# Kernel tuning notes

Hardware: AMD Instinct MI355X
Metric: run time of the kernel (lower is better)

The kernel has to match this reference:

```python
import jax, jax.numpy as jnp
import numpy as np

N_NODES = 50000
N_EDGES = 800000


def _gcn_conv(x, W, b, src, dst, deg_inv_sqrt, n_nodes):
    # PyG GCNConv: h = x @ W, then symmetric-normalized sum aggregation
    h = x @ W  # [N, F_out]
    norm = deg_inv_sqrt[src] * deg_inv_sqrt[dst]  # [E_aug]
    msg = h[src] * norm[:, None]  # [E_aug, F_out]
    out = jax.ops.segment_sum(msg, dst, num_segments=n_nodes)
    return out + b


def setup_inputs() -> dict:
    key = jax.random.key(0)
    k1, k2, k3, k4 = jax.random.split(key, 4)
    x = jax.random.normal(k1, (N_NODES, 128), dtype=jnp.float32)
    edge_index = jax.random.randint(k2, (2, N_EDGES), 0, N_NODES, dtype=jnp.int64)
    W1 = jax.random.normal(k3, (128, 64), dtype=jnp.float32) * (1.0 / np.sqrt(128))
    b1 = jnp.zeros((64,), dtype=jnp.float32)
    W2 = jax.random.normal(k4, (64, 32), dtype=jnp.float32) * (1.0 / np.sqrt(64))
    b2 = jnp.zeros((32,), dtype=jnp.float32)
    return {"x": x, "edge_index": edge_index, "W1": W1, "b1": b1, "W2": W2, "b2": b2}


def reference(x, edge_index, W1, b1, W2, b2):
    n_nodes = x.shape[0]
    # add self-loops (PyG GCNConv default)
    loop = jnp.arange(n_nodes, dtype=edge_index.dtype)
    src = jnp.concatenate([edge_index[0], loop])
    dst = jnp.concatenate([edge_index[1], loop])
    # symmetric normalization: deg from target index (gcn_norm)
    deg = jax.ops.segment_sum(jnp.ones_like(dst, dtype=x.dtype), dst, num_segments=n_nodes)
    deg_inv_sqrt = jnp.where(deg > 0, jax.lax.rsqrt(jnp.maximum(deg, 1.0)), 0.0)

    h = _gcn_conv(x, W1, b1, src, dst, deg_inv_sqrt, n_nodes)
    h = jax.nn.relu(h)
    # dropout is identity in eval mode (reference runs inference)
    out = _gcn_conv(h, W2, b2, src, dst, deg_inv_sqrt, n_nodes)
    return out
```

## Files before the change

kernel.cpp:

```cpp
#include <hip/hip_runtime.h>


#define F_IN 128
#define F_MID 64
#define F_OUT 32
#define NBLK 256

#define RFL(x) __builtin_amdgcn_readfirstlane(x)

__global__ __launch_bounds__(256) void k_hist(
    const int* __restrict__ dst, int E, int chunk, int nbuk,
    int* __restrict__ blockHist) {
    __shared__ int cnt[256];
    int t = threadIdx.x;
    cnt[t] = 0;
    __syncthreads();
    int e0 = blockIdx.x * chunk;
    int e1 = min(E, e0 + chunk);
    for (int e = e0 + t; e < e1; e += 256)
        atomicAdd(&cnt[dst[e] >> 8], 1);
    __syncthreads();
    if (t < nbuk) blockHist[blockIdx.x * nbuk + t] = cnt[t];
}

__global__ __launch_bounds__(256) void k_hist_scan(
    const int* __restrict__ blockHist, int nbuk,
    int* __restrict__ blockOff, int* __restrict__ bucketStart) {
    __shared__ int s[256];
    int t = threadIdx.x;
    int total = 0;
    if (t < nbuk)
        for (int blk = 0; blk < NBLK; ++blk) total += blockHist[blk * nbuk + t];
    s[t] = total;
    __syncthreads();
    for (int o = 1; o < 256; o <<= 1) {
        int add = (t >= o) ? s[t - o] : 0;
        __syncthreads();
        s[t] += add;
        __syncthreads();
    }
    int ex = s[t] - total;
    if (t < nbuk) {
        bucketStart[t] = ex;
        if (t == nbuk - 1) bucketStart[nbuk] = s[t];
        int running = ex;
        for (int blk = 0; blk < NBLK; ++blk) {
            blockOff[blk * nbuk + t] = running;
            running += blockHist[blk * nbuk + t];
        }
    }
}

__global__ __launch_bounds__(256) void k_scatter_edges(
    const int* __restrict__ src, const int* __restrict__ dst, int E, int chunk,
    int nbuk, const int* __restrict__ blockOff, int2* __restrict__ esort) {
    __shared__ int off[256];
    int t = threadIdx.x;
    if (t < nbuk) off[t] = blockOff[blockIdx.x * nbuk + t];
    __syncthreads();
    int e0 = blockIdx.x * chunk;
    int e1 = min(E, e0 + chunk);
    for (int e = e0 + t; e < e1; e += 256) {
        int d = dst[e];
        int pos = atomicAdd(&off[d >> 8], 1);
        esort[pos] = make_int2(d, src[e]);
    }
}

__global__ __launch_bounds__(256) void k_bucket_csr(
    const int2* __restrict__ esort, const int* __restrict__ bucketStart, int n,
    int* __restrict__ rowstart, int* __restrict__ deg, float* __restrict__ dis,
    int* __restrict__ col) {
    __shared__ int cnt[256];
    __shared__ int s[256];
    __shared__ int cur[256];
    int b = blockIdx.x;
    int t = threadIdx.x;
    int node0 = b << 8;
    int e0 = bucketStart[b], e1 = bucketStart[b + 1];
    cnt[t] = 0;
    __syncthreads();
    for (int e = e0 + t; e < e1; e += 256)
        atomicAdd(&cnt[esort[e].x & 255], 1);
    __syncthreads();
    int v = cnt[t];
    s[t] = v;
    __syncthreads();
    for (int o = 1; o < 256; o <<= 1) {
        int add = (t >= o) ? s[t - o] : 0;
        __syncthreads();
        s[t] += add;
        __syncthreads();
    }
    int ex = s[t] - v;
    cur[t] = ex;
    int node = node0 + t;
    if (node < n) {
        rowstart[node] = e0 + ex;
        deg[node] = v;
        dis[node] = rsqrtf((float)(v + 1));
    }
    __syncthreads();
    for (int e = e0 + t; e < e1; e += 256) {
        int2 p = esort[e];
        int pos = atomicAdd(&cur[p.x & 255], 1);
        col[e0 + pos] = p.y;
    }
}

__global__ __launch_bounds__(256, 4) void k_gemm1(
    const float* __restrict__ x, const float* __restrict__ W1,
    const float* __restrict__ dis, float* __restrict__ g1, int n) {
    __shared__ float xs[64 * 129];
    int tid  = threadIdx.x;
    int row0 = blockIdx.x * 64;
    for (int i = tid; i < 64 * F_IN; i += 256) {
        int r = i >> 7, k = i & 127;
        int gr = row0 + r;
        xs[r * 129 + k] = (gr < n) ? x[(size_t)gr * F_IN + k] : 0.0f;
    }
    __syncthreads();
    int w = RFL(tid >> 6);
    int r = tid & 63;
    const float4* W4 = (const float4*)W1;
    float4 a0 = {0.f,0.f,0.f,0.f}, a1 = a0, a2 = a0, a3 = a0;
#pragma unroll 4
    for (int k = 0; k < F_IN; ++k) {
        float xv = xs[r * 129 + k];
        float4 w0 = W4[k * 16 + w * 4 + 0];
        float4 w1 = W4[k * 16 + w * 4 + 1];
        float4 w2 = W4[k * 16 + w * 4 + 2];
        float4 w3 = W4[k * 16 + w * 4 + 3];
        a0.x += xv * w0.x; a0.y += xv * w0.y; a0.z += xv * w0.z; a0.w += xv * w0.w;
        a1.x += xv * w1.x; a1.y += xv * w1.y; a1.z += xv * w1.z; a1.w += xv * w1.w;
        a2.x += xv * w2.x; a2.y += xv * w2.y; a2.z += xv * w2.z; a2.w += xv * w2.w;
        a3.x += xv * w3.x; a3.y += xv * w3.y; a3.z += xv * w3.z; a3.w += xv * w3.w;
    }
    int gr = row0 + r;
    if (gr < n) {
        float dv = dis[gr];
        a0.x *= dv; a0.y *= dv; a0.z *= dv; a0.w *= dv;
        a1.x *= dv; a1.y *= dv; a1.z *= dv; a1.w *= dv;
        a2.x *= dv; a2.y *= dv; a2.z *= dv; a2.w *= dv;
        a3.x *= dv; a3.y *= dv; a3.z *= dv; a3.w *= dv;
        float4* o4 = (float4*)&g1[(size_t)gr * F_MID + w * 16];
        o4[0] = a0; o4[1] = a1; o4[2] = a2; o4[3] = a3;
    }
}

__global__ __launch_bounds__(256) void k_gather1(
    const int* __restrict__ rowstart, const int* __restrict__ deg,
    const int* __restrict__ col, const float* __restrict__ g1,
    const float* __restrict__ dis, const float* __restrict__ b1,
    float* __restrict__ h, int n) {
    int wave = RFL(threadIdx.x >> 6);
    int f    = threadIdx.x & 63;
    int d    = blockIdx.x * 4 + wave;
    if (d >= n) return;
    int base = RFL(rowstart[d]);
    int cnt  = RFL(deg[d]);
    float a0 = g1[(size_t)d * F_MID + f];
    float a1 = 0.f, a2 = 0.f, a3 = 0.f, a4 = 0.f, a5 = 0.f, a6 = 0.f, a7 = 0.f;
    int j = 0;
    for (; j + 8 <= cnt; j += 8) {
        int s0 = col[base + j + 0], s1 = col[base + j + 1];
        int s2 = col[base + j + 2], s3 = col[base + j + 3];
        int s4 = col[base + j + 4], s5 = col[base + j + 5];
        int s6 = col[base + j + 6], s7 = col[base + j + 7];
        a0 += g1[(size_t)s0 * F_MID + f];
        a1 += g1[(size_t)s1 * F_MID + f];
        a2 += g1[(size_t)s2 * F_MID + f];
        a3 += g1[(size_t)s3 * F_MID + f];
        a4 += g1[(size_t)s4 * F_MID + f];
        a5 += g1[(size_t)s5 * F_MID + f];
        a6 += g1[(size_t)s6 * F_MID + f];
        a7 += g1[(size_t)s7 * F_MID + f];
    }
    for (; j + 4 <= cnt; j += 4) {
        int s0 = col[base + j + 0], s1 = col[base + j + 1];
        int s2 = col[base + j + 2], s3 = col[base + j + 3];
        a0 += g1[(size_t)s0 * F_MID + f];
        a1 += g1[(size_t)s1 * F_MID + f];
        a2 += g1[(size_t)s2 * F_MID + f];
        a3 += g1[(size_t)s3 * F_MID + f];
    }
    for (; j < cnt; ++j) a0 += g1[(size_t)col[base + j] * F_MID + f];
    float acc = ((a0 + a1) + (a2 + a3)) + ((a4 + a5) + (a6 + a7));
    h[(size_t)d * F_MID + f] = fmaxf(acc * dis[d] + b1[f], 0.0f);
}

__global__ __launch_bounds__(256, 4) void k_gemm2(
    const float* __restrict__ h, const float* __restrict__ W2,
    const float* __restrict__ dis, float* __restrict__ g2, int n) {
    __shared__ float hs[64 * 65];
    int tid  = threadIdx.x;
    int row0 = blockIdx.x * 64;
    for (int i = tid; i < 64 * F_MID; i += 256) {
        int r = i >> 6, k = i & 63;
        int gr = row0 + r;
        hs[r * 65 + k] = (gr < n) ? h[(size_t)gr * F_MID + k] : 0.0f;
    }
    __syncthreads();
    int w = RFL(tid >> 6);
    int r = tid & 63;
    const float4* W4 = (const float4*)W2;
    float4 a0 = {0.f,0.f,0.f,0.f}, a1 = a0;
#pragma unroll 4
    for (int k = 0; k < F_MID; ++k) {
        float hv = hs[r * 65 + k];
        float4 w0 = W4[k * 8 + w * 2 + 0];
        float4 w1 = W4[k * 8 + w * 2 + 1];
        a0.x += hv * w0.x; a0.y += hv * w0.y; a0.z += hv * w0.z; a0.w += hv * w0.w;
        a1.x += hv * w1.x; a1.y += hv * w1.y; a1.z += hv * w1.z; a1.w += hv * w1.w;
    }
    int gr = row0 + r;
    if (gr < n) {
        float dv = dis[gr];
        a0.x *= dv; a0.y *= dv; a0.z *= dv; a0.w *= dv;
        a1.x *= dv; a1.y *= dv; a1.z *= dv; a1.w *= dv;
        float4* o4 = (float4*)&g2[(size_t)gr * F_OUT + w * 8];
        o4[0] = a0; o4[1] = a1;
    }
}

__global__ __launch_bounds__(256) void k_gather2(
    const int* __restrict__ rowstart, const int* __restrict__ deg,
    const int* __restrict__ col, const float* __restrict__ g2,
    const float* __restrict__ dis, const float* __restrict__ b2,
    float* __restrict__ out, int n) {
    int wave = RFL(threadIdx.x >> 6);
    int lane = threadIdx.x & 63;
    int j    = lane & 31;
    int p    = lane >> 5;
    int d    = blockIdx.x * 4 + wave;
    if (d >= n) return;
    int base = RFL(rowstart[d]);
    int cnt  = RFL(deg[d]);
    float a0 = (p == 0) ? g2[(size_t)d * F_OUT + j] : 0.0f;
    float a1 = 0.f, a2 = 0.f, a3 = 0.f;
    int t = 0;
    for (; t + 8 <= cnt; t += 8) {
        int sA0 = col[base + t + 0], sA1 = col[base + t + 1];
        int sB0 = col[base + t + 2], sB1 = col[base + t + 3];
        int sC0 = col[base + t + 4], sC1 = col[base + t + 5];
        int sD0 = col[base + t + 6], sD1 = col[base + t + 7];
        int sA = p ? sA1 : sA0;
        int sB = p ? sB1 : sB0;
        int sC = p ? sC1 : sC0;
        int sD = p ? sD1 : sD0;
        a0 += g2[(size_t)sA * F_OUT + j];
        a1 += g2[(size_t)sB * F_OUT + j];
        a2 += g2[(size_t)sC * F_OUT + j];
        a3 += g2[(size_t)sD * F_OUT + j];
    }
    for (; t + 2 <= cnt; t += 2) {
        int s0 = col[base + t], s1 = col[base + t + 1];
        int s = p ? s1 : s0;
        a0 += g2[(size_t)s * F_OUT + j];
    }
    if (t < cnt) {
        int s = col[base + t];
        if (p == 0) a0 += g2[(size_t)s * F_OUT + j];
    }
    float acc = (a0 + a1) + (a2 + a3);
    acc += __shfl_xor(acc, 32);
    if (p == 0) out[(size_t)d * F_OUT + j] = acc * dis[d] + b2[j];
}

extern "C" void kernel_launch(void* const* d_in, const int* in_sizes, int n_in,
                              void* d_out, int out_size, void* d_ws, size_t ws_size,
                              hipStream_t stream) {
    const float* x  = (const float*)d_in[0];
    const int*   ei = (const int*)d_in[1];
    const float* W1 = (const float*)d_in[2];
    const float* b1 = (const float*)d_in[3];
    const float* W2 = (const float*)d_in[4];
    const float* b2 = (const float*)d_in[5];

    int n = in_sizes[0] / F_IN;
    int E = in_sizes[1] / 2;
    const int* src = ei;
    const int* dst = ei + E;

    int nbuk  = (n + 255) >> 8;
    int chunk = (E + NBLK - 1) / NBLK;

    char* ws = (char*)d_ws;
    size_t off = 0;
    auto alloc = [&](size_t bytes) {
        char* p = ws + off;
        off += (bytes + 255) & ~(size_t)255;
        return p;
    };
    int*   blockHist   = (int*)  alloc((size_t)NBLK * nbuk * 4);
    int*   blockOff    = (int*)  alloc((size_t)NBLK * nbuk * 4);
    int*   bucketStart = (int*)  alloc((size_t)(nbuk + 1) * 4);
    int2*  esort       = (int2*) alloc((size_t)E * 8);
    int*   col         = (int*)  alloc((size_t)E * 4);
    int*   rowstart    = (int*)  alloc((size_t)n * 4);
    int*   deg         = (int*)  alloc((size_t)n * 4);
    float* dis         = (float*)alloc((size_t)n * 4);
    float* g1          = (float*)alloc((size_t)n * F_MID * 4);
    float* h           = (float*)alloc((size_t)n * F_MID * 4);
    float* g2          = (float*)alloc((size_t)n * F_OUT * 4);

    k_hist<<<NBLK, 256, 0, stream>>>(dst, E, chunk, nbuk, blockHist);
    k_hist_scan<<<1, 256, 0, stream>>>(blockHist, nbuk, blockOff, bucketStart);
    k_scatter_edges<<<NBLK, 256, 0, stream>>>(src, dst, E, chunk, nbuk, blockOff, esort);
    k_bucket_csr<<<nbuk, 256, 0, stream>>>(esort, bucketStart, n, rowstart, deg, dis, col);

    k_gemm1<<<(n + 63) / 64, 256, 0, stream>>>(x, W1, dis, g1, n);
    k_gather1<<<(n + 3) / 4, 256, 0, stream>>>(rowstart, deg, col, g1, dis, b1, h, n);
    k_gemm2<<<(n + 63) / 64, 256, 0, stream>>>(h, W2, dis, g2, n);
    k_gather2<<<(n + 3) / 4, 256, 0, stream>>>(rowstart, deg, col, g2, dis, b2,
                                               (float*)d_out, n);
}
```

Before: 208.7 us.

## Parallelize bucket offset scan across blocks instead of single serial block

```diff
diff --git a/kernel.cpp b/kernel.cpp
--- a/kernel.cpp
+++ b/kernel.cpp
@@ -23,15 +23,32 @@
     if (t < nbuk) blockHist[blockIdx.x * nbuk + t] = cnt[t];
 }
 
-__global__ __launch_bounds__(256) void k_hist_scan(
+__global__ __launch_bounds__(NBLK) void k_scan_buckets(
     const int* __restrict__ blockHist, int nbuk,
-    int* __restrict__ blockOff, int* __restrict__ bucketStart) {
+    int* __restrict__ blockOff, int* __restrict__ bucketTotal) {
+    __shared__ int s[NBLK];
+    int b = blockIdx.x;
+    int t = threadIdx.x;
+    int v = blockHist[t * nbuk + b];
+    s[t] = v;
+    __syncthreads();
+    for (int o = 1; o < NBLK; o <<= 1) {
+        int add = (t >= o) ? s[t - o] : 0;
+        __syncthreads();
+        s[t] += add;
+        __syncthreads();
+    }
+    blockOff[t * nbuk + b] = s[t] - v;
+    if (t == NBLK - 1) bucketTotal[b] = s[t];
+}
+
+__global__ __launch_bounds__(256) void k_scan_starts(
+    const int* __restrict__ bucketTotal, int nbuk, int E,
+    int* __restrict__ bucketStart) {
     __shared__ int s[256];
     int t = threadIdx.x;
-    int total = 0;
-    if (t < nbuk)
-        for (int blk = 0; blk < NBLK; ++blk) total += blockHist[blk * nbuk + t];
-    s[t] = total;
+    int v = (t < nbuk) ? bucketTotal[t] : 0;
+    s[t] = v;
     __syncthreads();
     for (int o = 1; o < 256; o <<= 1) {
         int add = (t >= o) ? s[t - o] : 0;
@@ -39,24 +56,17 @@
         s[t] += add;
         __syncthreads();
     }
-    int ex = s[t] - total;
-    if (t < nbuk) {
-        bucketStart[t] = ex;
-        if (t == nbuk - 1) bucketStart[nbuk] = s[t];
-        int running = ex;
-        for (int blk = 0; blk < NBLK; ++blk) {
-            blockOff[blk * nbuk + t] = running;
-            running += blockHist[blk * nbuk + t];
-        }
-    }
+    if (t < nbuk) bucketStart[t] = s[t] - v;
+    if (t == 0) bucketStart[nbuk] = E;
 }
 
 __global__ __launch_bounds__(256) void k_scatter_edges(
     const int* __restrict__ src, const int* __restrict__ dst, int E, int chunk,
-    int nbuk, const int* __restrict__ blockOff, int2* __restrict__ esort) {
+    int nbuk, const int* __restrict__ blockOff, const int* __restrict__ bucketStart,
+    int2* __restrict__ esort) {
     __shared__ int off[256];
     int t = threadIdx.x;
-    if (t < nbuk) off[t] = blockOff[blockIdx.x * nbuk + t];
+    if (t < nbuk) off[t] = blockOff[blockIdx.x * nbuk + t] + bucketStart[t];
     __syncthreads();
     int e0 = blockIdx.x * chunk;
     int e1 = min(E, e0 + chunk);
@@ -294,6 +304,7 @@
     };
     int*   blockHist   = (int*)  alloc((size_t)NBLK * nbuk * 4);
     int*   blockOff    = (int*)  alloc((size_t)NBLK * nbuk * 4);
+    int*   bucketTotal = (int*)  alloc((size_t)nbuk * 4);
     int*   bucketStart = (int*)  alloc((size_t)(nbuk + 1) * 4);
     int2*  esort       = (int2*) alloc((size_t)E * 8);
     int*   col         = (int*)  alloc((size_t)E * 4);
@@ -305,8 +316,10 @@
     float* g2          = (float*)alloc((size_t)n * F_OUT * 4);
 
     k_hist<<<NBLK, 256, 0, stream>>>(dst, E, chunk, nbuk, blockHist);
-    k_hist_scan<<<1, 256, 0, stream>>>(blockHist, nbuk, blockOff, bucketStart);
-    k_scatter_edges<<<NBLK, 256, 0, stream>>>(src, dst, E, chunk, nbuk, blockOff, esort);
+    k_scan_buckets<<<nbuk, NBLK, 0, stream>>>(blockHist, nbuk, blockOff, bucketTotal);
+    k_scan_starts<<<1, 256, 0, stream>>>(bucketTotal, nbuk, E, bucketStart);
+    k_scatter_edges<<<NBLK, 256, 0, stream>>>(src, dst, E, chunk, nbuk, blockOff,
+                                              bucketStart, esort);
     k_bucket_csr<<<nbuk, 256, 0, stream>>>(esort, bucketStart, n, rowstart, deg, dis, col);
 
     k_gemm1<<<(n + 63) / 64, 256, 0, stream>>>(x, W1, dis, g1, n);
```

Measured after the change: 198.9 us. 1.05x faster.
